# Kernel optimization log

Hardware: AMD Instinct MI355X
Metric: run time of the kernel (lower is better)

The kernel has to match this reference:

```python
import jax, jax.numpy as jnp
import numpy as np

NR, NL, K, TOPK, C, B = 4096, 16384, 8, 10, 16, 4
W_OCC, W_MDN, W_INT = 0.2, 1.0, 0.1
LOG2PI = float(np.log(2.0 * np.pi))


def setup_inputs() -> dict:
    key = jax.random.key(0)
    ks = jax.random.split(key, 12)
    radar_indices = jnp.concatenate([
        jax.random.randint(ks[0], (NR, 1), 0, B),
        jax.random.randint(ks[1], (NR, 1), 0, 41),
        jax.random.randint(ks[2], (NR, 2), 0, 176),
    ], axis=1).astype(jnp.int32)
    lidar_indices = jnp.concatenate([
        jax.random.randint(ks[3], (NL, 1), 0, B),
        jax.random.randint(ks[4], (NL, 1), 0, 41),
        jax.random.randint(ks[5], (NL, 2), 0, 176),
    ], axis=1).astype(jnp.int32)
    return {
        'mu_off': jax.random.normal(ks[6], (NR, K, 3)) * 2.0,
        'log_sig_off': jax.random.normal(ks[7], (NR, K, 3)) * 0.3,
        'mu_int': jax.random.normal(ks[8], (NR, K, 1)),
        'occ_logit': jax.random.normal(ks[9], (NR, K, 1)),
        'mix_logit': jax.random.normal(ks[10], (NR, K, 1)),
        'lidar_features': jax.random.normal(ks[11], (NL, C)),
        'radar_indices': radar_indices,
        'lidar_indices': lidar_indices,
        'gt_topk': TOPK,
    }


def _match(radar_indices, lidar_indices, topk):
    # per-batch top-k nearest lidar voxels for each radar voxel (vectorized:
    # dense masked distance matrix replaces the per-batch python loop)
    rb, lb = radar_indices[:, 0], lidar_indices[:, 0]
    rpos = radar_indices[:, 1:].astype(jnp.float32)  # (Nr,3) zyx
    lpos = lidar_indices[:, 1:].astype(jnp.float32)  # (Nl,3)
    d2 = ((rpos * rpos).sum(-1)[:, None] + (lpos * lpos).sum(-1)[None, :]
          - 2.0 * (rpos @ lpos.T))  # (Nr,Nl) squared dist, same order as cdist
    same = rb[:, None] == lb[None, :]
    d2 = jnp.where(same, d2, jnp.inf)  # cross-batch pairs excluded
    _, nn_idx = jax.lax.top_k(-d2, topk)  # (Nr,topk) smallest distances
    matched = same.any(axis=1)  # (Nr,)
    offs_zyx = (lidar_indices[nn_idx, 1:]
                - radar_indices[:, None, 1:]).astype(jnp.float32)  # (Nr,topk,3)
    offs_zyx = jnp.where(matched[:, None, None], offs_zyx, 0.0)
    return matched, nn_idx, offs_zyx


def reference(mu_off, log_sig_off, mu_int, occ_logit, mix_logit,
              lidar_features, radar_indices, lidar_indices, gt_topk):
    matched, nn_idx, offs_zyx = _match(radar_indices, lidar_indices, gt_topk)
    gt_feat = jnp.where(matched[:, None, None], lidar_features[nn_idx], 0.0)  # (Nr,T,C)
    y = offs_zyx[..., ::-1]  # flip zyx -> xyz, (Nr,T,3)

    # occupancy BCE-with-logits against matched mask
    occ_any = occ_logit[..., 0].max(axis=1)  # (Nr,)
    tgt = matched.astype(occ_any.dtype)
    occ_loss = (tgt * jax.nn.softplus(-occ_any)
                + (1.0 - tgt) * jax.nn.softplus(occ_any)).mean()

    # MDN log-prob: (Nr,T,K) mixture components
    log_pi = jax.nn.log_softmax(mix_logit[..., 0], axis=1)  # (Nr,K)
    mu_ = mu_off[:, None, :, :]       # (Nr,1,K,3)
    ls_ = log_sig_off[:, None, :, :]
    sigma2 = jnp.exp(2.0 * ls_) + 1e-12
    y_ = y[:, :, None, :]             # (Nr,T,1,3)
    logN = -0.5 * (((y_ - mu_) ** 2) / sigma2 + 2.0 * ls_ + LOG2PI).sum(-1)  # (Nr,T,K)
    log_post = logN + log_pi[:, None, :]
    logp = jax.nn.logsumexp(log_post, axis=-1)  # (Nr,T)

    # masked means emulate boolean-index-then-mean over matched rows
    m = matched.astype(jnp.float32)
    cnt = m.sum()
    T = logp.shape[1]
    mdn_nll = -(logp * m[:, None]).sum() / (cnt * T)

    # intensity loss (C % 4 == 0 path)
    gt_int = gt_feat.reshape(gt_feat.shape[0], gt_feat.shape[1], C // 4, 4)[..., 3].mean(axis=2)  # (Nr,T)
    r = jax.nn.softmax(log_post, axis=-1)  # (Nr,T,K) responsibilities
    term = r * jnp.abs(mu_int[:, None, :, 0] - gt_int[:, :, None])  # (Nr,T,K)
    int_loss = (term * m[:, None, None]).sum() / (cnt * T * r.shape[-1])

    return W_OCC * occ_loss + W_MDN * mdn_nll + W_INT * int_loss
```

## Files before the change

### kernel.cpp

```cpp
#include <hip/hip_runtime.h>
#include <cstdint>

#define NRAD 4096
#define NLID 16384
#define KMIX 8
#define TOPK 10
#define CF   16
#define LOG2PI 1.8378770664093453f

static constexpr unsigned INF_D2 = 62851u;

__device__ __forceinline__ void insert_key(unsigned (&t)[TOPK], unsigned key) {
#pragma unroll
    for (int i = TOPK - 1; i >= 1; --i) {
        unsigned hi = key > t[i - 1] ? key : t[i - 1];
        t[i] = hi < t[i] ? hi : t[i];
    }
    t[0] = key < t[0] ? key : t[0];
}

__device__ __forceinline__ void merge10(unsigned (&t)[TOPK], int lane,
                                        unsigned& mine, unsigned& first, unsigned& tenth) {
#pragma unroll
    for (int r = 0; r < TOPK; ++r) {
        unsigned v = t[0];
#pragma unroll
        for (int off = 32; off >= 1; off >>= 1) {
            unsigned o = __shfl_xor(v, off, 64);
            v = o < v ? o : v;
        }
        if (t[0] == v) {
#pragma unroll
            for (int i = 0; i < TOPK - 1; ++i) t[i] = t[i + 1];
            t[TOPK - 1] = 0xFFFFFFFFu;
        }
        if (lane == r) mine = v;
        if (r == 0) first = v;
        if (r == TOPK - 1) tenth = v;
    }
}

__device__ __forceinline__ float waveReduceSum(float v) {
#pragma unroll
    for (int off = 32; off >= 1; off >>= 1) v += __shfl_down(v, off, 64);
    return v;
}

__global__ __launch_bounds__(256) void prep_kernel(
        const int* __restrict__ lidar_indices,
        unsigned* __restrict__ packed_full,
        uint2* __restrict__ compacted,
        int* __restrict__ cursor) {
    int i = blockIdx.x * 256 + threadIdx.x;
    int lane = threadIdx.x & 63;
    int4 li = ((const int4*)lidar_indices)[i];
    int b = li.x;
    unsigned pos = ((unsigned)li.y << 16) | ((unsigned)li.z << 8) | (unsigned)li.w;
    packed_full[i] = ((unsigned)b << 22) | pos;
#pragma unroll
    for (int b2 = 0; b2 < 4; ++b2) {
        unsigned long long mask = __ballot(b == b2);
        if (b == b2) {
            int leader = __ffsll(mask) - 1;
            int off = (int)__popcll(mask & ((1ull << lane) - 1ull));
            int s = 0;
            if (lane == leader) s = atomicAdd(&cursor[b2], (int)__popcll(mask));
            s = __shfl(s, leader, 64);
            compacted[b2 * NLID + s + off] = make_uint2(pos, (unsigned)i);
        }
    }
}

__global__ __launch_bounds__(256) void topk_kernel(
        const uint2* __restrict__ compacted,
        const unsigned* __restrict__ packed_full,
        const int* __restrict__ cursor,
        const int* __restrict__ radar_indices,
        int* __restrict__ nn_out, int* __restrict__ matched_out) {
    int lane = threadIdx.x & 63;
    int row  = blockIdx.x * 4 + (threadIdx.x >> 6);
    int4 ri = ((const int4*)radar_indices)[row];
    int rb = ri.x, rz = ri.y, ry = ri.z, rx = ri.w;
    int c_cnt = cursor[rb];

    unsigned t[TOPK];
#pragma unroll
    for (int i = 0; i < TOPK; ++i) t[i] = 0xFFFFFFFFu;

    const uint4* src = (const uint4*)(compacted + rb * NLID);
    int iters = (c_cnt + 127) >> 7;
    uint4 q = src[lane];
    for (int it = 0; it < iters; ++it) {
        uint4 qn = q;
        if (it + 1 < iters) qn = src[(it + 1) * 64 + lane];
        int c0 = (it * 64 + lane) * 2;
        {
            int dz = (int)((q.x >> 16) & 63u)  - rz;
            int dy = (int)((q.x >> 8)  & 255u) - ry;
            int dx = (int)(q.x & 255u)         - rx;
            unsigned d2 = (unsigned)(dz * dz + dy * dy + dx * dx);
            unsigned key = (c0 < c_cnt) ? ((d2 << 14) | q.y) : 0xFFFFFFFFu;
            if (key < t[TOPK - 1]) insert_key(t, key);
        }
        {
            int dz = (int)((q.z >> 16) & 63u)  - rz;
            int dy = (int)((q.z >> 8)  & 255u) - ry;
            int dx = (int)(q.z & 255u)         - rx;
            unsigned d2 = (unsigned)(dz * dz + dy * dy + dx * dx);
            unsigned key = (c0 + 1 < c_cnt) ? ((d2 << 14) | q.w) : 0xFFFFFFFFu;
            if (key < t[TOPK - 1]) insert_key(t, key);
        }
        q = qn;
    }

    unsigned mine = 0, first = 0, tenth = 0;
    merge10(t, lane, mine, first, tenth);
    bool matched = true;

    if (tenth == 0xFFFFFFFFu) {
#pragma unroll
        for (int i = 0; i < TOPK; ++i) t[i] = 0xFFFFFFFFu;
        for (int it = 0; it < NLID / 256; ++it) {
            uint4 p4 = ((const uint4*)packed_full)[it * 64 + lane];
            unsigned base = it * 256 + lane * 4;
            unsigned ps[4] = {p4.x, p4.y, p4.z, p4.w};
#pragma unroll
            for (int j = 0; j < 4; ++j) {
                unsigned p = ps[j];
                int b  = (int)(p >> 22);
                int dz = (int)((p >> 16) & 63u)  - rz;
                int dy = (int)((p >> 8)  & 255u) - ry;
                int dx = (int)(p & 255u)         - rx;
                unsigned d2 = (unsigned)(dz * dz + dy * dy + dx * dx);
                unsigned hi = (b == rb) ? d2 : INF_D2;
                insert_key(t, (hi << 14) | (base + j));
            }
        }
        merge10(t, lane, mine, first, tenth);
        matched = first < (INF_D2 << 14);
    }

    if (lane < TOPK) nn_out[row * TOPK + lane] = (int)(mine & 0x3FFFu);
    if (lane == 0)   matched_out[row] = matched ? 1 : 0;
}

__global__ __launch_bounds__(256) void mdn_kernel(
        const float* __restrict__ mu_off, const float* __restrict__ log_sig_off,
        const float* __restrict__ mu_int, const float* __restrict__ occ_logit,
        const float* __restrict__ mix_logit, const float* __restrict__ lidar_features,
        const int* __restrict__ radar_indices, const int* __restrict__ lidar_indices,
        const int* __restrict__ nn, const int* __restrict__ matched,
        float* __restrict__ accum,
        unsigned* __restrict__ dctr,
        float* __restrict__ out) {
    int gid = blockIdx.x * 256 + threadIdx.x;
    int n  = gid / TOPK;
    int tt = gid - n * TOPK;
    int m  = matched[n];
    float mf = (float)m;
    int nni = nn[gid];

    int4 ri = ((const int4*)radar_indices)[n];
    int4 li = ((const int4*)lidar_indices)[nni];
    float y0 = mf * (float)(li.w - ri.w);
    float y1 = mf * (float)(li.z - ri.z);
    float y2 = mf * (float)(li.y - ri.y);

    float mix[KMIX];
    float mmax = -1e30f;
#pragma unroll
    for (int k = 0; k < KMIX; ++k) {
        mix[k] = mix_logit[n * KMIX + k];
        mmax = fmaxf(mmax, mix[k]);
    }
    float msum = 0.f;
#pragma unroll
    for (int k = 0; k < KMIX; ++k) msum += expf(mix[k] - mmax);
    float logZ = mmax + logf(msum);

    float lpost[KMIX];
    float pmax = -1e30f;
#pragma unroll
    for (int k = 0; k < KMIX; ++k) {
        int bidx = (n * KMIX + k) * 3;
        float mu0 = mu_off[bidx + 0], mu1 = mu_off[bidx + 1], mu2 = mu_off[bidx + 2];
        float l0 = log_sig_off[bidx + 0], l1 = log_sig_off[bidx + 1], l2 = log_sig_off[bidx + 2];
        float s0 = expf(2.f * l0) + 1e-12f;
        float s1 = expf(2.f * l1) + 1e-12f;
        float s2 = expf(2.f * l2) + 1e-12f;
        float d0 = y0 - mu0, d1 = y1 - mu1, d2v = y2 - mu2;
        float q = d0 * d0 / s0 + d1 * d1 / s1 + d2v * d2v / s2
                + 2.f * (l0 + l1 + l2) + 3.f * LOG2PI;
        lpost[k] = -0.5f * q + (mix[k] - logZ);
        pmax = fmaxf(pmax, lpost[k]);
    }
    float ex[KMIX];
    float se = 0.f;
#pragma unroll
    for (int k = 0; k < KMIX; ++k) { ex[k] = expf(lpost[k] - pmax); se += ex[k]; }
    float logp = pmax + logf(se);

    float gt = 0.f;
    if (m) {
        const float* lf = lidar_features + nni * CF;
        gt = 0.25f * (lf[3] + lf[7] + lf[11] + lf[15]);
    }
    float inv_se = 1.f / se;
    float isum = 0.f;
#pragma unroll
    for (int k = 0; k < KMIX; ++k)
        isum += ex[k] * inv_se * fabsf(mu_int[n * KMIX + k] - gt);

    float lp = mf * logp;
    float ip = mf * isum;
    float oc = 0.f, mc = 0.f;
    if (tt == 0) {
        float oa = -1e30f;
#pragma unroll
        for (int k = 0; k < KMIX; ++k) oa = fmaxf(oa, occ_logit[n * KMIX + k]);
        float soft_abs = log1pf(expf(-fabsf(oa)));
        oc = mf * (soft_abs + fmaxf(-oa, 0.f)) + (1.f - mf) * (soft_abs + fmaxf(oa, 0.f));
        mc = mf;
    }

    lp = waveReduceSum(lp); ip = waveReduceSum(ip);
    oc = waveReduceSum(oc); mc = waveReduceSum(mc);
    __shared__ float sA[4], sB[4], sC[4], sD[4];
    int wid = threadIdx.x >> 6, lane = threadIdx.x & 63;
    if (lane == 0) { sA[wid] = lp; sB[wid] = ip; sC[wid] = oc; sD[wid] = mc; }
    __syncthreads();
    if (threadIdx.x == 0) {
        atomicAdd(&accum[0], sA[0] + sA[1] + sA[2] + sA[3]);
        atomicAdd(&accum[1], sB[0] + sB[1] + sB[2] + sB[3]);
        atomicAdd(&accum[2], sC[0] + sC[1] + sC[2] + sC[3]);
        atomicAdd(&accum[3], sD[0] + sD[1] + sD[2] + sD[3]);
        __threadfence();
        unsigned done = atomicAdd(dctr, 1u);
        if (done == gridDim.x - 1) {
            __threadfence();
            float a = __hip_atomic_load(&accum[0], __ATOMIC_RELAXED, __HIP_MEMORY_SCOPE_AGENT);
            float b = __hip_atomic_load(&accum[1], __ATOMIC_RELAXED, __HIP_MEMORY_SCOPE_AGENT);
            float c = __hip_atomic_load(&accum[2], __ATOMIC_RELAXED, __HIP_MEMORY_SCOPE_AGENT);
            float d = __hip_atomic_load(&accum[3], __ATOMIC_RELAXED, __HIP_MEMORY_SCOPE_AGENT);
            float occ_loss = c / (float)NRAD;
            float mdn_nll  = -a / (d * (float)TOPK);
            float int_loss = b / (d * (float)TOPK * (float)KMIX);
            out[0] = 0.2f * occ_loss + mdn_nll + 0.1f * int_loss;
        }
    }
}

extern "C" void kernel_launch(void* const* d_in, const int* in_sizes, int n_in,
                              void* d_out, int out_size, void* d_ws, size_t ws_size,
                              hipStream_t stream) {
    const float* mu_off         = (const float*)d_in[0];
    const float* log_sig_off    = (const float*)d_in[1];
    const float* mu_int         = (const float*)d_in[2];
    const float* occ_logit      = (const float*)d_in[3];
    const float* mix_logit      = (const float*)d_in[4];
    const float* lidar_features = (const float*)d_in[5];
    const int*   radar_indices  = (const int*)d_in[6];
    const int*   lidar_indices  = (const int*)d_in[7];
    float* out = (float*)d_out;

    char* ws = (char*)d_ws;
    unsigned* packed_full = (unsigned*)(ws + 0);
    uint2*    compacted   = (uint2*)(ws + 65536);
    int*      cursor      = (int*)(ws + 589824);
    float*    accum       = (float*)(ws + 589840);
    unsigned* dctr        = (unsigned*)(ws + 589856);
    int*      nn          = (int*)(ws + 589888);
    int*      matched     = (int*)(ws + 753728);

    hipMemsetAsync(ws + 589824, 0, 64, stream);

    hipLaunchKernelGGL(prep_kernel, dim3(NLID / 256), dim3(256), 0, stream,
                       lidar_indices, packed_full, compacted, cursor);
    hipLaunchKernelGGL(topk_kernel, dim3(NRAD / 4), dim3(256), 0, stream,
                       compacted, packed_full, cursor, radar_indices, nn, matched);
    hipLaunchKernelGGL(mdn_kernel, dim3(NRAD * TOPK / 256), dim3(256), 0, stream,
                       mu_off, log_sig_off, mu_int, occ_logit, mix_logit,
                       lidar_features, radar_indices, lidar_indices,
                       nn, matched, accum, dctr, out);
}
```

Baseline: 121.8 us.

## Fuse prep, top-k and MDN stages into one cooperative grid-synced kernel

Replaces the three kernel launches with a single cooperative kernel of 512 persistent blocks. Lidar compaction runs first, then a grid sync, then each wavefront does the top-k search and evaluates the MDN loss directly on lanes 0-9, so the nn/matched buffers never go through global memory. The final reduction now uses per-block partials instead of global float atomics, and fast __expf/__logf intrinsics replace the precise math calls. In exchange it adds a grid-wide barrier, uses only 10 of 64 lanes during the MDN stage, and falls back to a two-kernel path if the cooperative launch fails.

```diff
diff --git a/kernel.cpp b/kernel.cpp
--- a/kernel.cpp
+++ b/kernel.cpp
@@ -1,5 +1,8 @@
 #include <hip/hip_runtime.h>
+#include <hip/hip_cooperative_groups.h>
 #include <cstdint>
+
+namespace cg = cooperative_groups;
 
 #define NRAD 4096
 #define NLID 16384
@@ -7,6 +10,7 @@
 #define TOPK 10
 #define CF   16
 #define LOG2PI 1.8378770664093453f
+#define GRID_BLOCKS 512
 
 static constexpr unsigned INF_D2 = 62851u;
 
@@ -46,208 +50,240 @@
     return v;
 }
 
-__global__ __launch_bounds__(256) void prep_kernel(
-        const int* __restrict__ lidar_indices,
-        unsigned* __restrict__ packed_full,
-        uint2* __restrict__ compacted,
-        int* __restrict__ cursor) {
-    int i = blockIdx.x * 256 + threadIdx.x;
-    int lane = threadIdx.x & 63;
-    int4 li = ((const int4*)lidar_indices)[i];
-    int b = li.x;
-    unsigned pos = ((unsigned)li.y << 16) | ((unsigned)li.z << 8) | (unsigned)li.w;
-    packed_full[i] = ((unsigned)b << 22) | pos;
-#pragma unroll
-    for (int b2 = 0; b2 < 4; ++b2) {
-        unsigned long long mask = __ballot(b == b2);
-        if (b == b2) {
-            int leader = __ffsll(mask) - 1;
-            int off = (int)__popcll(mask & ((1ull << lane) - 1ull));
-            int s = 0;
-            if (lane == leader) s = atomicAdd(&cursor[b2], (int)__popcll(mask));
-            s = __shfl(s, leader, 64);
-            compacted[b2 * NLID + s + off] = make_uint2(pos, (unsigned)i);
-        }
-    }
-}
-
-__global__ __launch_bounds__(256) void topk_kernel(
-        const uint2* __restrict__ compacted,
-        const unsigned* __restrict__ packed_full,
-        const int* __restrict__ cursor,
-        const int* __restrict__ radar_indices,
-        int* __restrict__ nn_out, int* __restrict__ matched_out) {
-    int lane = threadIdx.x & 63;
-    int row  = blockIdx.x * 4 + (threadIdx.x >> 6);
-    int4 ri = ((const int4*)radar_indices)[row];
-    int rb = ri.x, rz = ri.y, ry = ri.z, rx = ri.w;
-    int c_cnt = cursor[rb];
-
-    unsigned t[TOPK];
-#pragma unroll
-    for (int i = 0; i < TOPK; ++i) t[i] = 0xFFFFFFFFu;
-
-    const uint4* src = (const uint4*)(compacted + rb * NLID);
-    int iters = (c_cnt + 127) >> 7;
-    uint4 q = src[lane];
-    for (int it = 0; it < iters; ++it) {
-        uint4 qn = q;
-        if (it + 1 < iters) qn = src[(it + 1) * 64 + lane];
-        int c0 = (it * 64 + lane) * 2;
-        {
-            int dz = (int)((q.x >> 16) & 63u)  - rz;
-            int dy = (int)((q.x >> 8)  & 255u) - ry;
-            int dx = (int)(q.x & 255u)         - rx;
-            unsigned d2 = (unsigned)(dz * dz + dy * dy + dx * dx);
-            unsigned key = (c0 < c_cnt) ? ((d2 << 14) | q.y) : 0xFFFFFFFFu;
-            if (key < t[TOPK - 1]) insert_key(t, key);
-        }
-        {
-            int dz = (int)((q.z >> 16) & 63u)  - rz;
-            int dy = (int)((q.z >> 8)  & 255u) - ry;
-            int dx = (int)(q.z & 255u)         - rx;
-            unsigned d2 = (unsigned)(dz * dz + dy * dy + dx * dx);
-            unsigned key = (c0 + 1 < c_cnt) ? ((d2 << 14) | q.w) : 0xFFFFFFFFu;
-            if (key < t[TOPK - 1]) insert_key(t, key);
-        }
-        q = qn;
-    }
-
-    unsigned mine = 0, first = 0, tenth = 0;
-    merge10(t, lane, mine, first, tenth);
-    bool matched = true;
-
-    if (tenth == 0xFFFFFFFFu) {
-#pragma unroll
-        for (int i = 0; i < TOPK; ++i) t[i] = 0xFFFFFFFFu;
-        for (int it = 0; it < NLID / 256; ++it) {
-            uint4 p4 = ((const uint4*)packed_full)[it * 64 + lane];
-            unsigned base = it * 256 + lane * 4;
-            unsigned ps[4] = {p4.x, p4.y, p4.z, p4.w};
-#pragma unroll
-            for (int j = 0; j < 4; ++j) {
-                unsigned p = ps[j];
-                int b  = (int)(p >> 22);
-                int dz = (int)((p >> 16) & 63u)  - rz;
-                int dy = (int)((p >> 8)  & 255u) - ry;
-                int dx = (int)(p & 255u)         - rx;
-                unsigned d2 = (unsigned)(dz * dz + dy * dy + dx * dx);
-                unsigned hi = (b == rb) ? d2 : INF_D2;
-                insert_key(t, (hi << 14) | (base + j));
-            }
-        }
-        merge10(t, lane, mine, first, tenth);
-        matched = first < (INF_D2 << 14);
-    }
-
-    if (lane < TOPK) nn_out[row * TOPK + lane] = (int)(mine & 0x3FFFu);
-    if (lane == 0)   matched_out[row] = matched ? 1 : 0;
-}
-
-__global__ __launch_bounds__(256) void mdn_kernel(
+__device__ __forceinline__ void phaseA(const int* __restrict__ lidar_indices,
+                                       unsigned* __restrict__ packed_full,
+                                       uint2* __restrict__ compacted,
+                                       int* __restrict__ cursor, int nblocks) {
+    int tid = threadIdx.x, lane = tid & 63;
+    for (int base = blockIdx.x * 256; base < NLID; base += nblocks * 256) {
+        int i = base + tid;
+        int4 li = ((const int4*)lidar_indices)[i];
+        int b = li.x;
+        unsigned pos = ((unsigned)li.y << 16) | ((unsigned)li.z << 8) | (unsigned)li.w;
+        packed_full[i] = ((unsigned)b << 22) | pos;
+#pragma unroll
+        for (int b2 = 0; b2 < 4; ++b2) {
+            unsigned long long mask = __ballot(b == b2);
+            if (b == b2) {
+                int leader = __ffsll(mask) - 1;
+                int off = (int)__popcll(mask & ((1ull << lane) - 1ull));
+                int s = 0;
+                if (lane == leader) s = atomicAdd(&cursor[b2], (int)__popcll(mask));
+                s = __shfl(s, leader, 64);
+                compacted[b2 * NLID + s + off] = make_uint2(pos, (unsigned)i);
+            }
+        }
+    }
+}
+
+__device__ __forceinline__ void phaseBCD(
         const float* __restrict__ mu_off, const float* __restrict__ log_sig_off,
         const float* __restrict__ mu_int, const float* __restrict__ occ_logit,
         const float* __restrict__ mix_logit, const float* __restrict__ lidar_features,
         const int* __restrict__ radar_indices, const int* __restrict__ lidar_indices,
-        const int* __restrict__ nn, const int* __restrict__ matched,
-        float* __restrict__ accum,
-        unsigned* __restrict__ dctr,
-        float* __restrict__ out) {
-    int gid = blockIdx.x * 256 + threadIdx.x;
-    int n  = gid / TOPK;
-    int tt = gid - n * TOPK;
-    int m  = matched[n];
-    float mf = (float)m;
-    int nni = nn[gid];
-
-    int4 ri = ((const int4*)radar_indices)[n];
-    int4 li = ((const int4*)lidar_indices)[nni];
-    float y0 = mf * (float)(li.w - ri.w);
-    float y1 = mf * (float)(li.z - ri.z);
-    float y2 = mf * (float)(li.y - ri.y);
-
-    float mix[KMIX];
-    float mmax = -1e30f;
-#pragma unroll
-    for (int k = 0; k < KMIX; ++k) {
-        mix[k] = mix_logit[n * KMIX + k];
-        mmax = fmaxf(mmax, mix[k]);
-    }
-    float msum = 0.f;
-#pragma unroll
-    for (int k = 0; k < KMIX; ++k) msum += expf(mix[k] - mmax);
-    float logZ = mmax + logf(msum);
-
-    float lpost[KMIX];
-    float pmax = -1e30f;
-#pragma unroll
-    for (int k = 0; k < KMIX; ++k) {
-        int bidx = (n * KMIX + k) * 3;
-        float mu0 = mu_off[bidx + 0], mu1 = mu_off[bidx + 1], mu2 = mu_off[bidx + 2];
-        float l0 = log_sig_off[bidx + 0], l1 = log_sig_off[bidx + 1], l2 = log_sig_off[bidx + 2];
-        float s0 = expf(2.f * l0) + 1e-12f;
-        float s1 = expf(2.f * l1) + 1e-12f;
-        float s2 = expf(2.f * l2) + 1e-12f;
-        float d0 = y0 - mu0, d1 = y1 - mu1, d2v = y2 - mu2;
-        float q = d0 * d0 / s0 + d1 * d1 / s1 + d2v * d2v / s2
-                + 2.f * (l0 + l1 + l2) + 3.f * LOG2PI;
-        lpost[k] = -0.5f * q + (mix[k] - logZ);
-        pmax = fmaxf(pmax, lpost[k]);
-    }
-    float ex[KMIX];
-    float se = 0.f;
-#pragma unroll
-    for (int k = 0; k < KMIX; ++k) { ex[k] = expf(lpost[k] - pmax); se += ex[k]; }
-    float logp = pmax + logf(se);
-
-    float gt = 0.f;
-    if (m) {
-        const float* lf = lidar_features + nni * CF;
-        gt = 0.25f * (lf[3] + lf[7] + lf[11] + lf[15]);
-    }
-    float inv_se = 1.f / se;
-    float isum = 0.f;
-#pragma unroll
-    for (int k = 0; k < KMIX; ++k)
-        isum += ex[k] * inv_se * fabsf(mu_int[n * KMIX + k] - gt);
-
-    float lp = mf * logp;
-    float ip = mf * isum;
-    float oc = 0.f, mc = 0.f;
-    if (tt == 0) {
-        float oa = -1e30f;
-#pragma unroll
-        for (int k = 0; k < KMIX; ++k) oa = fmaxf(oa, occ_logit[n * KMIX + k]);
-        float soft_abs = log1pf(expf(-fabsf(oa)));
-        oc = mf * (soft_abs + fmaxf(-oa, 0.f)) + (1.f - mf) * (soft_abs + fmaxf(oa, 0.f));
-        mc = mf;
+        const uint2* __restrict__ compacted, const unsigned* __restrict__ packed_full,
+        const int* __restrict__ cursor, float4* __restrict__ partials,
+        unsigned* __restrict__ dctr, float* __restrict__ out, int nblocks) {
+    int tid = threadIdx.x, lane = tid & 63, wid = tid >> 6;
+    float lp = 0.f, ip = 0.f, oc = 0.f, mc = 0.f;
+
+    for (int row = blockIdx.x * 4 + wid; row < NRAD; row += nblocks * 4) {
+        int4 ri = ((const int4*)radar_indices)[row];
+        int rb = ri.x, rz = ri.y, ry = ri.z, rx = ri.w;
+        int c_cnt = cursor[rb];
+
+        unsigned t[TOPK];
+#pragma unroll
+        for (int i = 0; i < TOPK; ++i) t[i] = 0xFFFFFFFFu;
+
+        const uint4* src = (const uint4*)(compacted + rb * NLID);
+        int iters = (c_cnt + 127) >> 7;
+        uint4 q = src[lane];
+        for (int it = 0; it < iters; ++it) {
+            uint4 qn = q;
+            if (it + 1 < iters) qn = src[(it + 1) * 64 + lane];
+            int c0 = (it * 64 + lane) * 2;
+            {
+                int dz = (int)((q.x >> 16) & 63u)  - rz;
+                int dy = (int)((q.x >> 8)  & 255u) - ry;
+                int dx = (int)(q.x & 255u)         - rx;
+                unsigned d2 = (unsigned)(dz * dz + dy * dy + dx * dx);
+                unsigned key = (c0 < c_cnt) ? ((d2 << 14) | q.y) : 0xFFFFFFFFu;
+                if (key < t[TOPK - 1]) insert_key(t, key);
+            }
+            {
+                int dz = (int)((q.z >> 16) & 63u)  - rz;
+                int dy = (int)((q.z >> 8)  & 255u) - ry;
+                int dx = (int)(q.z & 255u)         - rx;
+                unsigned d2 = (unsigned)(dz * dz + dy * dy + dx * dx);
+                unsigned key = (c0 + 1 < c_cnt) ? ((d2 << 14) | q.w) : 0xFFFFFFFFu;
+                if (key < t[TOPK - 1]) insert_key(t, key);
+            }
+            q = qn;
+        }
+
+        unsigned mine = 0, first = 0, tenth = 0;
+        merge10(t, lane, mine, first, tenth);
+        bool matched = true;
+
+        if (tenth == 0xFFFFFFFFu) {
+#pragma unroll
+            for (int i = 0; i < TOPK; ++i) t[i] = 0xFFFFFFFFu;
+            for (int it = 0; it < NLID / 256; ++it) {
+                uint4 p4 = ((const uint4*)packed_full)[it * 64 + lane];
+                unsigned base = it * 256 + lane * 4;
+                unsigned ps[4] = {p4.x, p4.y, p4.z, p4.w};
+#pragma unroll
+                for (int j = 0; j < 4; ++j) {
+                    unsigned p = ps[j];
+                    int b  = (int)(p >> 22);
+                    int dz = (int)((p >> 16) & 63u)  - rz;
+                    int dy = (int)((p >> 8)  & 255u) - ry;
+                    int dx = (int)(p & 255u)         - rx;
+                    unsigned d2 = (unsigned)(dz * dz + dy * dy + dx * dx);
+                    unsigned hi = (b == rb) ? d2 : INF_D2;
+                    insert_key(t, (hi << 14) | (base + j));
+                }
+            }
+            merge10(t, lane, mine, first, tenth);
+            matched = first < (INF_D2 << 14);
+        }
+
+        float mf = matched ? 1.f : 0.f;
+        if (lane < TOPK) {
+            int nni = (int)(mine & 0x3FFFu);
+            int4 ll = ((const int4*)lidar_indices)[nni];
+            float y0 = mf * (float)(ll.w - rx);
+            float y1 = mf * (float)(ll.z - ry);
+            float y2 = mf * (float)(ll.y - rz);
+
+            float mix[KMIX];
+            float mmax = -1e30f;
+#pragma unroll
+            for (int k = 0; k < KMIX; ++k) {
+                mix[k] = mix_logit[row * KMIX + k];
+                mmax = fmaxf(mmax, mix[k]);
+            }
+            float msum = 0.f;
+#pragma unroll
+            for (int k = 0; k < KMIX; ++k) msum += __expf(mix[k] - mmax);
+            float logZ = mmax + __logf(msum);
+
+            float lpost[KMIX];
+            float pmax = -1e30f;
+#pragma unroll
+            for (int k = 0; k < KMIX; ++k) {
+                int bidx = (row * KMIX + k) * 3;
+                float mu0 = mu_off[bidx + 0], mu1 = mu_off[bidx + 1], mu2 = mu_off[bidx + 2];
+                float l0 = log_sig_off[bidx + 0], l1 = log_sig_off[bidx + 1], l2 = log_sig_off[bidx + 2];
+                float s0 = __expf(2.f * l0) + 1e-12f;
+                float s1 = __expf(2.f * l1) + 1e-12f;
+                float s2 = __expf(2.f * l2) + 1e-12f;
+                float d0 = y0 - mu0, d1 = y1 - mu1, d2v = y2 - mu2;
+                float qq = d0 * d0 / s0 + d1 * d1 / s1 + d2v * d2v / s2
+                         + 2.f * (l0 + l1 + l2) + 3.f * LOG2PI;
+                lpost[k] = -0.5f * qq + (mix[k] - logZ);
+                pmax = fmaxf(pmax, lpost[k]);
+            }
+            float ex[KMIX];
+            float se = 0.f;
+#pragma unroll
+            for (int k = 0; k < KMIX; ++k) { ex[k] = __expf(lpost[k] - pmax); se += ex[k]; }
+            float logp = pmax + __logf(se);
+
+            float gt = 0.f;
+            if (matched) {
+                const float* lf = lidar_features + nni * CF;
+                gt = 0.25f * (lf[3] + lf[7] + lf[11] + lf[15]);
+            }
+            float inv_se = 1.f / se;
+            float isum = 0.f;
+#pragma unroll
+            for (int k = 0; k < KMIX; ++k)
+                isum += ex[k] * inv_se * fabsf(mu_int[row * KMIX + k] - gt);
+
+            lp += mf * logp;
+            ip += mf * isum;
+            if (lane == 0) {
+                float oa = -1e30f;
+#pragma unroll
+                for (int k = 0; k < KMIX; ++k) oa = fmaxf(oa, occ_logit[row * KMIX + k]);
+                float soft_abs = log1pf(__expf(-fabsf(oa)));
+                oc += mf * (soft_abs + fmaxf(-oa, 0.f)) + (1.f - mf) * (soft_abs + fmaxf(oa, 0.f));
+                mc += mf;
+            }
+        }
     }
 
     lp = waveReduceSum(lp); ip = waveReduceSum(ip);
     oc = waveReduceSum(oc); mc = waveReduceSum(mc);
     __shared__ float sA[4], sB[4], sC[4], sD[4];
-    int wid = threadIdx.x >> 6, lane = threadIdx.x & 63;
+    __shared__ int isLast;
     if (lane == 0) { sA[wid] = lp; sB[wid] = ip; sC[wid] = oc; sD[wid] = mc; }
     __syncthreads();
-    if (threadIdx.x == 0) {
-        atomicAdd(&accum[0], sA[0] + sA[1] + sA[2] + sA[3]);
-        atomicAdd(&accum[1], sB[0] + sB[1] + sB[2] + sB[3]);
-        atomicAdd(&accum[2], sC[0] + sC[1] + sC[2] + sC[3]);
-        atomicAdd(&accum[3], sD[0] + sD[1] + sD[2] + sD[3]);
+    if (tid == 0) {
+        partials[blockIdx.x] = make_float4(sA[0] + sA[1] + sA[2] + sA[3],
+                                           sB[0] + sB[1] + sB[2] + sB[3],
+                                           sC[0] + sC[1] + sC[2] + sC[3],
+                                           sD[0] + sD[1] + sD[2] + sD[3]);
         __threadfence();
         unsigned done = atomicAdd(dctr, 1u);
-        if (done == gridDim.x - 1) {
-            __threadfence();
-            float a = __hip_atomic_load(&accum[0], __ATOMIC_RELAXED, __HIP_MEMORY_SCOPE_AGENT);
-            float b = __hip_atomic_load(&accum[1], __ATOMIC_RELAXED, __HIP_MEMORY_SCOPE_AGENT);
-            float c = __hip_atomic_load(&accum[2], __ATOMIC_RELAXED, __HIP_MEMORY_SCOPE_AGENT);
-            float d = __hip_atomic_load(&accum[3], __ATOMIC_RELAXED, __HIP_MEMORY_SCOPE_AGENT);
+        isLast = (done == (unsigned)(nblocks - 1)) ? 1 : 0;
+    }
+    __syncthreads();
+    if (isLast) {
+        __threadfence();
+        float a = 0.f, b = 0.f, c = 0.f, d = 0.f;
+        for (int i = tid; i < nblocks; i += 256) {
+            float4 p = partials[i];
+            a += p.x; b += p.y; c += p.z; d += p.w;
+        }
+        a = waveReduceSum(a); b = waveReduceSum(b);
+        c = waveReduceSum(c); d = waveReduceSum(d);
+        if (lane == 0) { sA[wid] = a; sB[wid] = b; sC[wid] = c; sD[wid] = d; }
+        __syncthreads();
+        if (tid == 0) {
+            a = sA[0] + sA[1] + sA[2] + sA[3];
+            b = sB[0] + sB[1] + sB[2] + sB[3];
+            c = sC[0] + sC[1] + sC[2] + sC[3];
+            d = sD[0] + sD[1] + sD[2] + sD[3];
             float occ_loss = c / (float)NRAD;
             float mdn_nll  = -a / (d * (float)TOPK);
             float int_loss = b / (d * (float)TOPK * (float)KMIX);
             out[0] = 0.2f * occ_loss + mdn_nll + 0.1f * int_loss;
         }
     }
+}
+
+__global__ __launch_bounds__(256) void coop_kernel(
+        const float* mu_off, const float* log_sig_off, const float* mu_int,
+        const float* occ_logit, const float* mix_logit, const float* lidar_features,
+        const int* radar_indices, const int* lidar_indices,
+        unsigned* packed_full, uint2* compacted, int* cursor,
+        float4* partials, unsigned* dctr, float* out) {
+    phaseA(lidar_indices, packed_full, compacted, cursor, GRID_BLOCKS);
+    __threadfence();
+    cg::this_grid().sync();
+    phaseBCD(mu_off, log_sig_off, mu_int, occ_logit, mix_logit, lidar_features,
+             radar_indices, lidar_indices, compacted, packed_full, cursor,
+             partials, dctr, out, GRID_BLOCKS);
+}
+
+__global__ __launch_bounds__(256) void prep_kernel(
+        const int* __restrict__ lidar_indices, unsigned* __restrict__ packed_full,
+        uint2* __restrict__ compacted, int* __restrict__ cursor) {
+    phaseA(lidar_indices, packed_full, compacted, cursor, 64);
+}
+
+__global__ __launch_bounds__(256) void main_kernel(
+        const float* mu_off, const float* log_sig_off, const float* mu_int,
+        const float* occ_logit, const float* mix_logit, const float* lidar_features,
+        const int* radar_indices, const int* lidar_indices,
+        const unsigned* packed_full, const uint2* compacted, const int* cursor,
+        float4* partials, unsigned* dctr, float* out) {
+    phaseBCD(mu_off, log_sig_off, mu_int, occ_logit, mix_logit, lidar_features,
+             radar_indices, lidar_indices, compacted, packed_full, cursor,
+             partials, dctr, out, GRID_BLOCKS);
 }
 
 extern "C" void kernel_launch(void* const* d_in, const int* in_sizes, int n_in,
@@ -267,19 +303,26 @@
     unsigned* packed_full = (unsigned*)(ws + 0);
     uint2*    compacted   = (uint2*)(ws + 65536);
     int*      cursor      = (int*)(ws + 589824);
-    float*    accum       = (float*)(ws + 589840);
-    unsigned* dctr        = (unsigned*)(ws + 589856);
-    int*      nn          = (int*)(ws + 589888);
-    int*      matched     = (int*)(ws + 753728);
+    unsigned* dctr        = (unsigned*)(ws + 589840);
+    float4*   partials    = (float4*)(ws + 589888);
 
     hipMemsetAsync(ws + 589824, 0, 64, stream);
 
-    hipLaunchKernelGGL(prep_kernel, dim3(NLID / 256), dim3(256), 0, stream,
-                       lidar_indices, packed_full, compacted, cursor);
-    hipLaunchKernelGGL(topk_kernel, dim3(NRAD / 4), dim3(256), 0, stream,
-                       compacted, packed_full, cursor, radar_indices, nn, matched);
-    hipLaunchKernelGGL(mdn_kernel, dim3(NRAD * TOPK / 256), dim3(256), 0, stream,
-                       mu_off, log_sig_off, mu_int, occ_logit, mix_logit,
-                       lidar_features, radar_indices, lidar_indices,
-                       nn, matched, accum, dctr, out);
-}
+    void* args[] = {
+        (void*)&mu_off, (void*)&log_sig_off, (void*)&mu_int, (void*)&occ_logit,
+        (void*)&mix_logit, (void*)&lidar_features, (void*)&radar_indices,
+        (void*)&lidar_indices, (void*)&packed_full, (void*)&compacted,
+        (void*)&cursor, (void*)&partials, (void*)&dctr, (void*)&out
+    };
+    hipError_t e = hipLaunchCooperativeKernel((const void*)coop_kernel,
+                                              dim3(GRID_BLOCKS), dim3(256),
+                                              args, 0, stream);
+    if (e != hipSuccess) {
+        hipLaunchKernelGGL(prep_kernel, dim3(64), dim3(256), 0, stream,
+                           lidar_indices, packed_full, compacted, cursor);
+        hipLaunchKernelGGL(main_kernel, dim3(GRID_BLOCKS), dim3(256), 0, stream,
+                           mu_off, log_sig_off, mu_int, occ_logit, mix_logit,
+                           lidar_features, radar_indices, lidar_indices,
+                           packed_full, compacted, cursor, partials, dctr, out);
+    }
+}
```

Result: slower. 233.2 us (+91.4%).
